# Kernel optimization log

Hardware: AMD Instinct MI355X
Metric: run time of the kernel (lower is better)

Reference implementation:

```python
import jax, jax.numpy as jnp
import numpy as np
from jax import lax

B, T, F, H, NC = 64, 256, 64, 128, 2


def setup_inputs() -> dict:
    key = jax.random.key(0)
    ks = jax.random.split(key, 10)
    # timestamps: sorted ints with duplicates -> exercises per-timestamp mean aggregation
    t = jnp.sort(jax.random.randint(ks[0], (B, T), 0, T // 2), axis=1).astype(jnp.float32)
    m = jax.random.randint(ks[1], (B, T), 0, F).astype(jnp.float32)
    x = jax.random.normal(ks[2], (B, T), dtype=jnp.float32)
    delt = jax.random.uniform(ks[3], (B, T), dtype=jnp.float32)
    X = jnp.stack([t, m, x, delt], axis=1)  # [B, 4, T]
    lengths = jax.random.randint(ks[4], (B,), T // 2, T + 1).astype(jnp.int32)
    s = 1.0 / np.sqrt(H + 1)
    W_lin = jax.random.uniform(ks[5], (F, H + 1, 4 * H), minval=-s, maxval=s, dtype=jnp.float32)
    b_lin = jax.random.uniform(ks[6], (F, 4 * H), minval=-s, maxval=s, dtype=jnp.float32)
    W_dec = jax.random.uniform(ks[7], (F,), minval=-1.0, maxval=1.0, dtype=jnp.float32)
    b_dec = jax.random.uniform(ks[8], (F,), minval=-1.0, maxval=1.0, dtype=jnp.float32)
    so = 1.0 / np.sqrt(F * H + H)
    k9, k10 = jax.random.split(ks[9])
    W_out = jax.random.uniform(k9, (F * H + H, NC), minval=-so, maxval=so, dtype=jnp.float32)
    b_out = jax.random.uniform(k10, (NC,), minval=-so, maxval=so, dtype=jnp.float32)
    return {"X": X, "lengths": lengths, "W_lin": W_lin, "b_lin": b_lin,
            "W_dec": W_dec, "b_dec": b_dec, "W_out": W_out, "b_out": b_out}


def _forward(X, lengths, W_lin, b_lin, W_dec, b_dec, W_out, b_out):
    nF, Hp1, H4 = W_lin.shape
    hs = Hp1 - 1
    t = X[:, 0]
    m = X[:, 1].astype(jnp.int32)
    x = X[:, 2]
    delt = X[:, 3]
    idx = jnp.arange(t.shape[1])
    valid = idx[None, :] < lengths[:, None]                       # event is real
    t_next = jnp.concatenate([t[:, 1:], t[:, -1:] + 1.0], axis=1)
    # last event of a consecutive-equal-timestamp group (within valid length)
    boundary = (idx[None, :] == (lengths[:, None] - 1)) | (t_next != t)

    def per_sample(m_s, x_s, d_s, v_s, b_s):
        def step(carry, inp):
            h_t, c_t, acc, cnt = carry
            mj, xj, dj, vj, bj = inp
            # feature-specific decay of that feature's hidden row
            dm = W_dec[mj] * dj + b_dec[mj]
            decay = jnp.exp(-jnp.maximum(0.0, dm))
            h_dec = decay * h_t[mj]
            inp_vec = jnp.concatenate([xj[None], h_dec])          # [H+1]
            gates = inp_vec @ W_lin[mj] + b_lin[mj]               # [4H]
            gi, gf, go, gc = jnp.split(gates, 4)
            c_cand = jax.nn.sigmoid(gf) * c_t + jax.nn.sigmoid(gi) * jnp.tanh(gc)
            h_row = jax.nn.sigmoid(go) * jnp.tanh(c_cand)
            h_t = jnp.where(vj, h_t.at[mj].set(h_row), h_t)
            acc = acc + jnp.where(vj, c_cand, 0.0)
            cnt = cnt + jnp.where(vj, 1.0, 0.0)
            close = vj & bj                                       # end of timestamp group
            c_t = jnp.where(close, acc / jnp.maximum(cnt, 1.0), c_t)
            acc = jnp.where(close, jnp.zeros_like(acc), acc)
            cnt = jnp.where(close, 0.0, cnt)
            return (h_t, c_t, acc, cnt), None

        init = (jnp.zeros((nF, hs), jnp.float32), jnp.zeros((hs,), jnp.float32),
                jnp.zeros((hs,), jnp.float32), jnp.float32(0.0))
        (h_t, c_t, _, _), _ = lax.scan(step, init, (m_s, x_s, d_s, v_s, b_s))
        feats = jnp.concatenate([c_t, h_t.reshape(-1)])           # [H + F*H]
        return jax.nn.softmax(feats @ W_out + b_out)

    return jax.vmap(per_sample)(m, x, delt, valid, boundary)      # [B, n_class]


def reference(X, lengths, W_lin, b_lin, W_dec, b_dec, W_out, b_out):
    return _forward(X, lengths, W_lin, b_lin, W_dec, b_dec, W_out, b_out)
```

## Files before the change

kernel.cpp:

```cpp
#include <hip/hip_runtime.h>
#include <math.h>
#include <stdint.h>

#define BATCH 64
#define T 256
#define NF 64
#define H 128
#define H4 512
#define HP1 129
#define WF_STRIDE (HP1 * H4)
#define FEATS (NF * H + H)
#define NTH3 1024

#define PACK2_U4 (64 * 8 * 2 * 4 * 64)
#define PACK2_BYTES ((size_t)PACK2_U4 * 16u)
#define HDR2_BYTES  (64u * 512u * 16u)
#define WS_NEED ((size_t)HDR2_BYTES + PACK2_BYTES)

typedef float vf2 __attribute__((ext_vector_type(2)));

__device__ __forceinline__ float sigmoidf_(float x) {
    return 1.0f / (1.0f + __expf(-x));
}

__device__ __forceinline__ float tanhf_(float x) {
    float ax = fabsf(x);
    float e = __expf(2.0f * ax);
    float r = 1.0f - 2.0f / (e + 1.0f);
    return copysignf(r, x);
}

template<bool HI>
__device__ __forceinline__ vf2 dec2f(unsigned u) {
    return __builtin_amdgcn_cvt_pk_f32_fp8(u, HI);
}

__global__ __launch_bounds__(256)
void repack2_kernel(const float* __restrict__ W_lin, uint4* __restrict__ pack2) {
    const int lin = blockIdx.x * 256 + threadIdx.x;
    const int l   = lin & 63;
    const int i   = (lin >> 6) & 3;
    const int Xv  = (lin >> 8) & 1;
    const int wv  = (lin >> 9) & 7;
    const int f   = lin >> 12;
    const int h   = wv * 16 + (l & 15);
    const int ks  = l >> 4;
    const int g   = Xv * 2 + (i >> 1);
    const int ksub = i & 1;
    const int col = g * 128 + h;
    const int k0  = ks * 32 + ksub * 16;
    const float* src = W_lin + (size_t)f * WF_STRIDE + (size_t)(1 + k0) * H4 + col;
    unsigned u[4];
    #pragma unroll
    for (int dw = 0; dw < 4; ++dw) {
        const float v0 = src[(4 * dw + 0) * H4] * 4096.0f;
        const float v1 = src[(4 * dw + 1) * H4] * 4096.0f;
        const float v2 = src[(4 * dw + 2) * H4] * 4096.0f;
        const float v3 = src[(4 * dw + 3) * H4] * 4096.0f;
        unsigned r = 0;
        r = __builtin_amdgcn_cvt_pk_fp8_f32(v0, v1, r, false);
        r = __builtin_amdgcn_cvt_pk_fp8_f32(v2, v3, r, true);
        u[dw] = r;
    }
    uint4 o; o.x = u[0]; o.y = u[1]; o.z = u[2]; o.w = u[3];
    pack2[lin] = o;
}

__global__ __launch_bounds__(256)
void hdr2_kernel(const float* __restrict__ W_lin, const float* __restrict__ b_lin,
                 uint4* __restrict__ hdr2) {
    const int lin = blockIdx.x * 256 + threadIdx.x;
    const int t2 = lin & 511, f = lin >> 9;
    const int wv = t2 >> 6, l = t2 & 63;
    const int h  = wv * 16 + (l & 15);
    union { uint4 u; _Float16 hf[8]; } o;
    #pragma unroll
    for (int g = 0; g < 4; ++g) {
        o.hf[g]     = (_Float16)W_lin[(size_t)f * WF_STRIDE + g * 128 + h];
        o.hf[4 + g] = (_Float16)b_lin[f * H4 + g * 128 + h];
    }
    hdr2[lin] = o.u;
}

__global__ __launch_bounds__(NTH3, 4)
void lstm_scan_fp8_pair(const float* __restrict__ X,
                        const int* __restrict__ lengths,
                        const float* __restrict__ W_dec,
                        const float* __restrict__ b_dec,
                        const float* __restrict__ W_out,
                        const float* __restrict__ b_out,
                        const uint4* __restrict__ pack2,
                        const uint4* __restrict__ hdr2,
                        float* __restrict__ out)
{
    __shared__ float s_ht[NF * H];
    __shared__ float s_inpA[H];
    __shared__ float s_inpB[H];
    __shared__ float s_gates[2][H][4];
    __shared__ float s_X[4 * T];
    __shared__ float s_wdec[NF];
    __shared__ float s_bdec[NF];
    __shared__ float s_cfin[H];
    __shared__ float s_red[32];

    const int tid = threadIdx.x;
    const int b   = blockIdx.x;
    const int grp = tid >> 9;
    const int w8  = (tid >> 6) & 7;
    const int l   = tid & 63;
    const int h   = w8 * 16 + (l & 15);
    const int ks  = l >> 4;

    const float* Xb = X + b * 4 * T;
    const int len = lengths[b];

    for (int i = tid; i < NF * H; i += NTH3) s_ht[i] = 0.0f;
    for (int i = tid; i < 4 * T; i += NTH3) s_X[i] = Xb[i];
    if (tid < NF) { s_wdec[tid] = W_dec[tid]; s_bdec[tid] = b_dec[tid]; }
    if (tid < H) { s_inpA[tid] = 0.0f; s_inpB[tid] = 0.0f; }
    __syncthreads();

    float c_t = 0.0f, accv = 0.0f, cntv = 0.0f;

    #define DOTQ(Wq, G, KS) do {                                                \
        const int pb = (KS) * 8;                                                \
        vf2 d;                                                                  \
        d = dec2f<false>((Wq).x); acc[G] += d * iv[pb + 0];                     \
        d = dec2f<true >((Wq).x); acc[G] += d * iv[pb + 1];                     \
        d = dec2f<false>((Wq).y); acc[G] += d * iv[pb + 2];                     \
        d = dec2f<true >((Wq).y); acc[G] += d * iv[pb + 3];                     \
        d = dec2f<false>((Wq).z); acc[G] += d * iv[pb + 4];                     \
        d = dec2f<true >((Wq).z); acc[G] += d * iv[pb + 5];                     \
        d = dec2f<false>((Wq).w); acc[G] += d * iv[pb + 6];                     \
        d = dec2f<true >((Wq).w); acc[G] += d * iv[pb + 7];                     \
    } while (0)

    #define MATVEC(MF, INP, XV, GATE) do {                                      \
        uint4 q[8];                                                             \
        const uint4* wp_ = pack2 + (((size_t)(MF) * 8 + w8) * 2 * 4) * 64 + l;  \
        _Pragma("unroll")                                                       \
        for (int ii = 0; ii < 8; ++ii) q[ii] = wp_[ii * 64];                    \
        union { uint4 u; _Float16 hf[8]; } hu_;                                 \
        hu_.u = hdr2[(size_t)(MF) * 512 + (w8 * 64 + l)];                       \
        vf2 iv[16];                                                             \
        {                                                                       \
            const float4* ip_ = (const float4*)((INP) + ks * 32);               \
            _Pragma("unroll")                                                   \
            for (int qd = 0; qd < 8; ++qd) {                                    \
                const float4 t_ = ip_[qd];                                      \
                iv[2 * qd][0] = t_.x;     iv[2 * qd][1] = t_.y;                 \
                iv[2 * qd + 1][0] = t_.z; iv[2 * qd + 1][1] = t_.w;             \
            }                                                                   \
        }                                                                       \
        vf2 acc[4];                                                             \
        _Pragma("unroll")                                                       \
        for (int g = 0; g < 4; ++g) { acc[g][0] = 0.0f; acc[g][1] = 0.0f; }     \
        _Pragma("unroll")                                                       \
        for (int Xi = 0; Xi < 2; ++Xi) {                                        \
            DOTQ(q[Xi * 4 + 0], Xi * 2 + 0, 0);                                 \
            DOTQ(q[Xi * 4 + 1], Xi * 2 + 0, 1);                                 \
            DOTQ(q[Xi * 4 + 2], Xi * 2 + 1, 0);                                 \
            DOTQ(q[Xi * 4 + 3], Xi * 2 + 1, 1);                                 \
        }                                                                       \
        _Pragma("unroll")                                                       \
        for (int g = 0; g < 4; ++g) {                                           \
            float s_ = acc[g][0] + acc[g][1];                                   \
            s_ += __shfl_xor(s_, 16, 64);                                       \
            s_ += __shfl_xor(s_, 32, 64);                                       \
            GATE[g] = fmaf(s_, 1.0f / 4096.0f,                                  \
                           fmaf((XV), (float)hu_.hf[g], (float)hu_.hf[4 + g])); \
        }                                                                       \
    } while (0)

    for (int j = 0; j < len; j += 2) {
        const int  vj1 = (j + 1 < len);
        const int  mj  = (int)s_X[T + j];
        const int  j1c = (j + 1 < T) ? (j + 1) : (T - 1);
        const int  mj1 = (int)s_X[T + j1c];
        const float xj  = s_X[2 * T + j];
        const float xj1 = s_X[2 * T + j1c];

        {
            const int   myM   = grp ? mj1 : mj;
            const float myx   = grp ? xj1 : xj;
            const float* myin = grp ? s_inpB : s_inpA;
            float gate[4];
            MATVEC(myM, myin, myx, gate);
            if (ks == 0) {
                float4 g4; g4.x = gate[0]; g4.y = gate[1]; g4.z = gate[2]; g4.w = gate[3];
                *(float4*)&s_gates[grp][h][0] = g4;
            }
        }
        __syncthreads();

        const float4 gA = *(const float4*)&s_gates[0][h][0];
        float4 gB = *(const float4*)&s_gates[1][h][0];

        const float c_candA = sigmoidf_(gA.y) * c_t + sigmoidf_(gA.x) * tanhf_(gA.w);
        const float h_rowA  = sigmoidf_(gA.z) * tanhf_(c_candA);
        accv += c_candA;
        cntv += 1.0f;
        {
            const float tj  = s_X[j];
            const float tn1 = (j < T - 1) ? s_X[j + 1] : (tj + 1.0f);
            const bool bdry = (j == len - 1) || (tn1 != tj);
            if (bdry) { c_t = accv / fmaxf(cntv, 1.0f); accv = 0.0f; cntv = 0.0f; }
        }

        const bool coll = vj1 && (mj1 == mj);
        if (coll) {
            const float d1  = s_X[3 * T + j1c];
            const float dm1 = fmaf(s_wdec[mj1], d1, s_bdec[mj1]);
            const float de1 = __expf(-fmaxf(0.0f, dm1));
            if (grp == 1 && ks == 0) s_inpB[h] = de1 * h_rowA;
            __syncthreads();
            if (grp == 1) {
                float gr[4];
                MATVEC(mj1, s_inpB, xj1, gr);
                if (ks == 0) {
                    float4 g4; g4.x = gr[0]; g4.y = gr[1]; g4.z = gr[2]; g4.w = gr[3];
                    *(float4*)&s_gates[1][h][0] = g4;
                }
            }
            __syncthreads();
            gB = *(const float4*)&s_gates[1][h][0];
        }

        float h_rowB = 0.0f;
        if (vj1) {
            const float c_candB = sigmoidf_(gB.y) * c_t + sigmoidf_(gB.x) * tanhf_(gB.w);
            h_rowB = sigmoidf_(gB.z) * tanhf_(c_candB);
            accv += c_candB;
            cntv += 1.0f;
            const float tj1 = s_X[j1c];
            const float tn2 = (j + 1 < T - 1) ? s_X[j + 2] : (tj1 + 1.0f);
            const bool bdry = (j + 1 == len - 1) || (tn2 != tj1);
            if (bdry) { c_t = accv / fmaxf(cntv, 1.0f); accv = 0.0f; cntv = 0.0f; }
        }

        if (ks == 0) {
            if (grp == 0 && !coll) s_ht[mj * H + h] = h_rowA;
            if (grp == 1 && vj1)   s_ht[mj1 * H + h] = h_rowB;
        }

        const int j2 = (j + 2 < T) ? (j + 2) : (T - 1);
        const int j3 = (j + 3 < T) ? (j + 3) : (T - 1);
        const int m2 = (int)s_X[T + j2];
        const int m3 = (int)s_X[T + j3];
        if (ks == 0 && grp == 0) {
            const float d2  = s_X[3 * T + j2];
            const float dm2 = fmaf(s_wdec[m2], d2, s_bdec[m2]);
            const float de2 = __expf(-fmaxf(0.0f, dm2));
            const float hv2 = (vj1 && m2 == mj1) ? h_rowB
                            : ((m2 == mj) ? h_rowA : s_ht[m2 * H + h]);
            s_inpA[h] = de2 * hv2;
        }
        if (ks == 0 && grp == 1) {
            const float d3  = s_X[3 * T + j3];
            const float dm3 = fmaf(s_wdec[m3], d3, s_bdec[m3]);
            const float de3 = __expf(-fmaxf(0.0f, dm3));
            const float hv3 = (vj1 && m3 == mj1) ? h_rowB
                            : ((m3 == mj) ? h_rowA : s_ht[m3 * H + h]);
            s_inpB[h] = de3 * hv3;
        }
        __syncthreads();
    }
    #undef MATVEC
    #undef DOTQ

    if (grp == 0 && ks == 0) s_cfin[h] = c_t;
    __syncthreads();

    float z0 = 0.0f, z1 = 0.0f;
    for (int i = tid; i < FEATS; i += NTH3) {
        const float f = (i < H) ? s_cfin[i] : s_ht[i - H];
        const float2 wo = *(const float2*)(W_out + 2 * i);
        z0 = fmaf(f, wo.x, z0);
        z1 = fmaf(f, wo.y, z1);
    }
    #pragma unroll
    for (int off = 32; off > 0; off >>= 1) {
        z0 += __shfl_down(z0, off, 64);
        z1 += __shfl_down(z1, off, 64);
    }
    const int wave = tid >> 6, lane2 = tid & 63;
    if (lane2 == 0) { s_red[2 * wave] = z0; s_red[2 * wave + 1] = z1; }
    __syncthreads();
    if (tid == 0) {
        float a0 = b_out[0], a1 = b_out[1];
        #pragma unroll
        for (int q = 0; q < 16; ++q) { a0 += s_red[2 * q]; a1 += s_red[2 * q + 1]; }
        const float mx = fmaxf(a0, a1);
        const float e0 = __expf(a0 - mx), e1 = __expf(a1 - mx);
        const float inv = 1.0f / (e0 + e1);
        out[2 * b]     = e0 * inv;
        out[2 * b + 1] = e1 * inv;
    }
}

#define NTHREADS 512
__global__ __launch_bounds__(NTHREADS)
void lstm_scan_kernel(const float* __restrict__ X,
                      const int* __restrict__ lengths,
                      const float* __restrict__ W_lin,
                      const float* __restrict__ b_lin,
                      const float* __restrict__ W_dec,
                      const float* __restrict__ b_dec,
                      const float* __restrict__ W_out,
                      const float* __restrict__ b_out,
                      float* __restrict__ out)
{
    __shared__ float s_feats[FEATS];
    __shared__ float s_inp[H];
    __shared__ float s_part[4][H4];
    __shared__ float s_X[4 * T];
    __shared__ float s_wdec[NF];
    __shared__ float s_bdec[NF];
    __shared__ float s_red[16];

    float* s_ct = s_feats;
    float* s_ht = s_feats + H;

    const int tid = threadIdx.x;
    const int b   = blockIdx.x;
    const int g4  = tid & 127;
    const int kq  = tid >> 7;

    const float* Xb = X + b * 4 * T;
    const int len = lengths[b];

    for (int i = tid; i < NF * H; i += NTHREADS) s_ht[i] = 0.0f;
    for (int i = tid; i < 4 * T; i += NTHREADS) s_X[i] = Xb[i];
    if (tid < NF) { s_wdec[tid] = W_dec[tid]; s_bdec[tid] = b_dec[tid]; }
    __syncthreads();

    float c_t = 0.0f, acc = 0.0f, cnt = 0.0f;

    for (int j = 0; j < len; ++j) {
        const int   mj = (int)s_X[T + j];
        const float xj = s_X[2 * T + j];
        const float* Wf = W_lin + mj * WF_STRIDE;

        float bl0, bl1, bl2, bl3;
        if (tid < H) {
            const float dj    = s_X[3 * T + j];
            const float dm    = fmaf(s_wdec[mj], dj, s_bdec[mj]);
            const float decay = __expf(-fmaxf(0.0f, dm));
            s_inp[tid] = decay * s_ht[mj * H + tid];
            const int m4 = mj * H4;
            bl0 = b_lin[m4 + tid];
            bl1 = b_lin[m4 + H + tid];
            bl2 = b_lin[m4 + 2 * H + tid];
            bl3 = b_lin[m4 + 3 * H + tid];
        }
        __syncthreads();

        float4 a4 = make_float4(0.0f, 0.0f, 0.0f, 0.0f);
        {
            const float*  wr  = Wf + (1 + kq * 32) * H4 + 4 * g4;
            const float4* ivp = (const float4*)(s_inp + kq * 32);
            #pragma unroll
            for (int cc = 0; cc < 8; ++cc) {
                const float4 v = ivp[cc];
                const float* wrc = wr + (4 * cc) * H4;
                const float4 w0 = *(const float4*)(wrc);
                const float4 w1 = *(const float4*)(wrc + H4);
                const float4 w2 = *(const float4*)(wrc + 2 * H4);
                const float4 w3 = *(const float4*)(wrc + 3 * H4);
                a4.x = fmaf(v.x, w0.x, a4.x); a4.y = fmaf(v.x, w0.y, a4.y);
                a4.z = fmaf(v.x, w0.z, a4.z); a4.w = fmaf(v.x, w0.w, a4.w);
                a4.x = fmaf(v.y, w1.x, a4.x); a4.y = fmaf(v.y, w1.y, a4.y);
                a4.z = fmaf(v.y, w1.z, a4.z); a4.w = fmaf(v.y, w1.w, a4.w);
                a4.x = fmaf(v.z, w2.x, a4.x); a4.y = fmaf(v.z, w2.y, a4.y);
                a4.z = fmaf(v.z, w2.z, a4.z); a4.w = fmaf(v.z, w2.w, a4.w);
                a4.x = fmaf(v.w, w3.x, a4.x); a4.y = fmaf(v.w, w3.y, a4.y);
                a4.z = fmaf(v.w, w3.z, a4.z); a4.w = fmaf(v.w, w3.w, a4.w);
            }
        }
        if (kq == 0) {
            const float4 wv = *(const float4*)(Wf + 4 * g4);
            a4.x = fmaf(xj, wv.x, a4.x); a4.y = fmaf(xj, wv.y, a4.y);
            a4.z = fmaf(xj, wv.z, a4.z); a4.w = fmaf(xj, wv.w, a4.w);
        }
        *(float4*)(&s_part[kq][4 * g4]) = a4;
        __syncthreads();

        if (tid < H) {
            const int h = tid;
            const float gi = s_part[0][h]         + s_part[1][h]         + s_part[2][h]         + s_part[3][h]         + bl0;
            const float gf = s_part[0][H + h]     + s_part[1][H + h]     + s_part[2][H + h]     + s_part[3][H + h]     + bl1;
            const float go = s_part[0][2*H + h]   + s_part[1][2*H + h]   + s_part[2][2*H + h]   + s_part[3][2*H + h]   + bl2;
            const float gc = s_part[0][3*H + h]   + s_part[1][3*H + h]   + s_part[2][3*H + h]   + s_part[3][3*H + h]   + bl3;

            const float c_cand = sigmoidf_(gf) * c_t + sigmoidf_(gi) * tanhf_(gc);
            const float h_row  = sigmoidf_(go) * tanhf_(c_cand);
            s_ht[mj * H + h] = h_row;
            acc += c_cand;
            cnt += 1.0f;

            const float tj = s_X[j];
            const float tn = (j < T - 1) ? s_X[j + 1] : (tj + 1.0f);
            const bool boundary = (j == len - 1) || (tn != tj);
            if (boundary) { c_t = acc / fmaxf(cnt, 1.0f); acc = 0.0f; cnt = 0.0f; }
        }
        __syncthreads();
    }

    if (tid < H) s_ct[tid] = c_t;
    __syncthreads();

    float z0 = 0.0f, z1 = 0.0f;
    for (int i = tid; i < FEATS; i += NTHREADS) {
        const float f = s_feats[i];
        const float2 wv = *(const float2*)(W_out + 2 * i);
        z0 = fmaf(f, wv.x, z0);
        z1 = fmaf(f, wv.y, z1);
    }
    #pragma unroll
    for (int off = 32; off > 0; off >>= 1) {
        z0 += __shfl_down(z0, off, 64);
        z1 += __shfl_down(z1, off, 64);
    }
    const int wave = tid >> 6, lane = tid & 63;
    if (lane == 0) { s_red[2 * wave] = z0; s_red[2 * wave + 1] = z1; }
    __syncthreads();
    if (tid == 0) {
        float a0 = b_out[0], a1 = b_out[1];
        #pragma unroll
        for (int q = 0; q < 8; ++q) { a0 += s_red[2 * q]; a1 += s_red[2 * q + 1]; }
        const float mx = fmaxf(a0, a1);
        const float e0 = __expf(a0 - mx), e1 = __expf(a1 - mx);
        const float inv = 1.0f / (e0 + e1);
        out[2 * b]     = e0 * inv;
        out[2 * b + 1] = e1 * inv;
    }
}

extern "C" void kernel_launch(void* const* d_in, const int* in_sizes, int n_in,
                              void* d_out, int out_size, void* d_ws, size_t ws_size,
                              hipStream_t stream) {
    const float* X      = (const float*)d_in[0];
    const int*   lens   = (const int*)d_in[1];
    const float* W_lin  = (const float*)d_in[2];
    const float* b_lin  = (const float*)d_in[3];
    const float* W_dec  = (const float*)d_in[4];
    const float* b_dec  = (const float*)d_in[5];
    const float* W_out  = (const float*)d_in[6];
    const float* b_out  = (const float*)d_in[7];
    float* out = (float*)d_out;

    if (ws_size >= WS_NEED) {
        uint4* hdr2 = (uint4*)d_ws;
        uint4* pack2 = (uint4*)((char*)d_ws + HDR2_BYTES);
        hipLaunchKernelGGL(hdr2_kernel, dim3(128), dim3(256), 0, stream,
                           W_lin, b_lin, hdr2);
        hipLaunchKernelGGL(repack2_kernel, dim3(PACK2_U4 / 256), dim3(256), 0, stream,
                           W_lin, pack2);
        hipLaunchKernelGGL(lstm_scan_fp8_pair, dim3(BATCH), dim3(NTH3), 0, stream,
                           X, lens, W_dec, b_dec, W_out, b_out, pack2, hdr2, out);
    } else {
        hipLaunchKernelGGL(lstm_scan_kernel, dim3(BATCH), dim3(NTHREADS), 0, stream,
                           X, lens, W_lin, b_lin, W_dec, b_dec, W_out, b_out, out);
    }
}
```

Baseline: 542.8 us.

## Prefetch next-step FP8 weights into LDS via async global_load_lds

The scan kernel now issues asynchronous global-to-LDS loads (global_load_lds) for the next step's feature weight slice while the current step computes, then reads weights from LDS with ds_read_b128 instead of loading them from global memory on the critical path. The hidden-state table moves to fp16 so the 128 KB weight staging buffer fits in shared memory, and __syncthreads is replaced by hand-written waitcnt/barrier macros. The aim is to hide global-memory latency in the serial per-timestep recurrence. In exchange it uses much more LDS, adds fp16 rounding to the stored hidden states, and depends on hand-placed waitcnt ordering being correct.

New measurement: 572.4 us. +5.5%, slower.

```diff
diff --git a/kernel.cpp b/kernel.cpp
--- a/kernel.cpp
+++ b/kernel.cpp
@@ -10,7 +10,7 @@
 #define HP1 129
 #define WF_STRIDE (HP1 * H4)
 #define FEATS (NF * H + H)
-#define NTH3 1024
+#define NTH4 1024
 
 #define PACK2_U4 (64 * 8 * 2 * 4 * 64)
 #define PACK2_BYTES ((size_t)PACK2_U4 * 16u)
@@ -34,6 +34,21 @@
 __device__ __forceinline__ vf2 dec2f(unsigned u) {
     return __builtin_amdgcn_cvt_pk_f32_fp8(u, HI);
 }
+
+__device__ __forceinline__ void dma16(const void* g, uint32_t lds_byte) {
+    __builtin_amdgcn_global_load_lds(
+        (const __attribute__((address_space(1))) void*)g,
+        (__attribute__((address_space(3))) void*)(uintptr_t)lds_byte,
+        16, 0, 0);
+}
+
+#define WAITV0() do { asm volatile("s_waitcnt vmcnt(0)" ::: "memory"); \
+                      __builtin_amdgcn_sched_barrier(0); } while (0)
+#define LGKM0()  do { asm volatile("s_waitcnt lgkmcnt(0)" ::: "memory"); \
+                      __builtin_amdgcn_sched_barrier(0); } while (0)
+#define BARRIER() do { asm volatile("s_waitcnt lgkmcnt(0)" ::: "memory"); \
+                       __builtin_amdgcn_s_barrier(); \
+                       asm volatile("" ::: "memory"); } while (0)
 
 __global__ __launch_bounds__(256)
 void repack2_kernel(const float* __restrict__ W_lin, uint4* __restrict__ pack2) {
@@ -82,22 +97,23 @@
     hdr2[lin] = o.u;
 }
 
-__global__ __launch_bounds__(NTH3, 4)
-void lstm_scan_fp8_pair(const float* __restrict__ X,
-                        const int* __restrict__ lengths,
-                        const float* __restrict__ W_dec,
-                        const float* __restrict__ b_dec,
-                        const float* __restrict__ W_out,
-                        const float* __restrict__ b_out,
-                        const uint4* __restrict__ pack2,
-                        const uint4* __restrict__ hdr2,
-                        float* __restrict__ out)
+__global__ __launch_bounds__(NTH4, 4)
+void lstm_scan_fp8_pair2(const float* __restrict__ X,
+                         const int* __restrict__ lengths,
+                         const float* __restrict__ W_dec,
+                         const float* __restrict__ b_dec,
+                         const float* __restrict__ W_out,
+                         const float* __restrict__ b_out,
+                         const uint4* __restrict__ pack2,
+                         const uint4* __restrict__ hdr2,
+                         float* __restrict__ out)
 {
-    __shared__ float s_ht[NF * H];
+    __shared__ __align__(16) char s_wb[131072];
+    __shared__ _Float16 s_ht[NF * H];
+    __shared__ __align__(16) float s_gates[2][H][4];
+    __shared__ float s_X[4 * T];
     __shared__ float s_inpA[H];
     __shared__ float s_inpB[H];
-    __shared__ float s_gates[2][H][4];
-    __shared__ float s_X[4 * T];
     __shared__ float s_wdec[NF];
     __shared__ float s_bdec[NF];
     __shared__ float s_cfin[H];
@@ -114,13 +130,24 @@
     const float* Xb = X + b * 4 * T;
     const int len = lengths[b];
 
-    for (int i = tid; i < NF * H; i += NTH3) s_ht[i] = 0.0f;
-    for (int i = tid; i < 4 * T; i += NTH3) s_X[i] = Xb[i];
+    for (int i = tid; i < NF * H; i += NTH4) s_ht[i] = (_Float16)0.0f;
+    for (int i = tid; i < 4 * T; i += NTH4) s_X[i] = Xb[i];
     if (tid < NF) { s_wdec[tid] = W_dec[tid]; s_bdec[tid] = b_dec[tid]; }
     if (tid < H) { s_inpA[tid] = 0.0f; s_inpB[tid] = 0.0f; }
     __syncthreads();
 
+    const uint32_t wb0 = (uint32_t)(uintptr_t)s_wb;
+    const uint32_t slice = __builtin_amdgcn_readfirstlane(
+        wb0 + (uint32_t)grp * 65536u + (uint32_t)w8 * 8192u);
+
     float c_t = 0.0f, accv = 0.0f, cntv = 0.0f;
+
+    #define ISSUE8(MF) do {                                                     \
+        const uint4* gp_ = pack2 + ((size_t)(MF) * 8 + w8) * 512 + l;           \
+        _Pragma("unroll")                                                       \
+        for (int ii = 0; ii < 8; ++ii)                                          \
+            dma16(gp_ + ii * 64, slice + (uint32_t)(ii * 1024));                \
+    } while (0)
 
     #define DOTQ(Wq, G, KS) do {                                                \
         const int pb = (KS) * 8;                                                \
@@ -135,13 +162,22 @@
         d = dec2f<true >((Wq).w); acc[G] += d * iv[pb + 7];                     \
     } while (0)
 
-    #define MATVEC(MF, INP, XV, GATE) do {                                      \
-        uint4 q[8];                                                             \
-        const uint4* wp_ = pack2 + (((size_t)(MF) * 8 + w8) * 2 * 4) * 64 + l;  \
-        _Pragma("unroll")                                                       \
-        for (int ii = 0; ii < 8; ++ii) q[ii] = wp_[ii * 64];                    \
-        union { uint4 u; _Float16 hf[8]; } hu_;                                 \
-        hu_.u = hdr2[(size_t)(MF) * 512 + (w8 * 64 + l)];                       \
+    #define MATVEC_LDS(INP, XV, HU, GATE) do {                                  \
+        uint4 q0, q1, q2, q3, q4, q5, q6, q7;                                   \
+        const uint32_t ra_ = wb0 + (uint32_t)grp * 65536u                       \
+                           + (uint32_t)w8 * 8192u + (uint32_t)l * 16u;          \
+        asm volatile("ds_read_b128 %0, %4 offset:0\n\t"                         \
+                     "ds_read_b128 %1, %4 offset:1024\n\t"                      \
+                     "ds_read_b128 %2, %4 offset:2048\n\t"                      \
+                     "ds_read_b128 %3, %4 offset:3072"                          \
+                     : "=&v"(q0), "=&v"(q1), "=&v"(q2), "=&v"(q3)               \
+                     : "v"(ra_) : "memory");                                    \
+        asm volatile("ds_read_b128 %0, %4 offset:4096\n\t"                      \
+                     "ds_read_b128 %1, %4 offset:5120\n\t"                      \
+                     "ds_read_b128 %2, %4 offset:6144\n\t"                      \
+                     "ds_read_b128 %3, %4 offset:7168"                          \
+                     : "=&v"(q4), "=&v"(q5), "=&v"(q6), "=&v"(q7)               \
+                     : "v"(ra_) : "memory");                                    \
         vf2 iv[16];                                                             \
         {                                                                       \
             const float4* ip_ = (const float4*)((INP) + ks * 32);               \
@@ -152,25 +188,27 @@
                 iv[2 * qd + 1][0] = t_.z; iv[2 * qd + 1][1] = t_.w;             \
             }                                                                   \
         }                                                                       \
+        LGKM0();          \
         vf2 acc[4];                                                             \
         _Pragma("unroll")                                                       \
         for (int g = 0; g < 4; ++g) { acc[g][0] = 0.0f; acc[g][1] = 0.0f; }     \
-        _Pragma("unroll")                                                       \
-        for (int Xi = 0; Xi < 2; ++Xi) {                                        \
-            DOTQ(q[Xi * 4 + 0], Xi * 2 + 0, 0);                                 \
-            DOTQ(q[Xi * 4 + 1], Xi * 2 + 0, 1);                                 \
-            DOTQ(q[Xi * 4 + 2], Xi * 2 + 1, 0);                                 \
-            DOTQ(q[Xi * 4 + 3], Xi * 2 + 1, 1);                                 \
-        }                                                                       \
+        DOTQ(q0, 0, 0); DOTQ(q1, 0, 1); DOTQ(q2, 1, 0); DOTQ(q3, 1, 1);         \
+        DOTQ(q4, 2, 0); DOTQ(q5, 2, 1); DOTQ(q6, 3, 0); DOTQ(q7, 3, 1);         \
         _Pragma("unroll")                                                       \
         for (int g = 0; g < 4; ++g) {                                           \
             float s_ = acc[g][0] + acc[g][1];                                   \
             s_ += __shfl_xor(s_, 16, 64);                                       \
             s_ += __shfl_xor(s_, 32, 64);                                       \
             GATE[g] = fmaf(s_, 1.0f / 4096.0f,                                  \
-                           fmaf((XV), (float)hu_.hf[g], (float)hu_.hf[4 + g])); \
+                           fmaf((XV), (float)(HU).hf[g], (float)(HU).hf[4 + g])); \
         }                                                                       \
     } while (0)
+
+    {
+        const int m0 = (int)s_X[T];
+        const int m1 = (int)s_X[T + ((1 < T) ? 1 : (T - 1))];
+        ISSUE8(grp ? m1 : m0);
+    }
 
     for (int j = 0; j < len; j += 2) {
         const int  vj1 = (j + 1 < len);
@@ -179,19 +217,32 @@
         const int  mj1 = (int)s_X[T + j1c];
         const float xj  = s_X[2 * T + j];
         const float xj1 = s_X[2 * T + j1c];
-
-        {
-            const int   myM   = grp ? mj1 : mj;
-            const float myx   = grp ? xj1 : xj;
-            const float* myin = grp ? s_inpB : s_inpA;
-            float gate[4];
-            MATVEC(myM, myin, myx, gate);
-            if (ks == 0) {
-                float4 g4; g4.x = gate[0]; g4.y = gate[1]; g4.z = gate[2]; g4.w = gate[3];
-                *(float4*)&s_gates[grp][h][0] = g4;
-            }
-        }
-        __syncthreads();
+        const bool coll = vj1 && (mj1 == mj);
+        const int  j2 = (j + 2 < T) ? (j + 2) : (T - 1);
+        const int  j3 = (j + 3 < T) ? (j + 3) : (T - 1);
+        const int  m2 = (int)s_X[T + j2];
+        const int  m3 = (int)s_X[T + j3];
+
+        const int   myM   = grp ? mj1 : mj;
+        const float myx   = grp ? xj1 : xj;
+        const float* myin = grp ? s_inpB : s_inpA;
+
+        union { uint4 u; _Float16 hf[8]; } hu;
+        hu.u = hdr2[(size_t)myM * 512 + (w8 * 64 + l)];
+
+        WAITV0();
+
+        float gate[4];
+        MATVEC_LDS(myin, myx, hu, gate);
+
+        if (grp == 0) ISSUE8(m2);
+        else if (!coll) ISSUE8(m3);
+
+        if (ks == 0) {
+            float4 g4; g4.x = gate[0]; g4.y = gate[1]; g4.z = gate[2]; g4.w = gate[3];
+            *(float4*)&s_gates[grp][h][0] = g4;
+        }
+        BARRIER();
 
         const float4 gA = *(const float4*)&s_gates[0][h][0];
         float4 gB = *(const float4*)&s_gates[1][h][0];
@@ -207,22 +258,22 @@
             if (bdry) { c_t = accv / fmaxf(cntv, 1.0f); accv = 0.0f; cntv = 0.0f; }
         }
 
-        const bool coll = vj1 && (mj1 == mj);
         if (coll) {
             const float d1  = s_X[3 * T + j1c];
             const float dm1 = fmaf(s_wdec[mj1], d1, s_bdec[mj1]);
             const float de1 = __expf(-fmaxf(0.0f, dm1));
             if (grp == 1 && ks == 0) s_inpB[h] = de1 * h_rowA;
-            __syncthreads();
+            BARRIER();
             if (grp == 1) {
                 float gr[4];
-                MATVEC(mj1, s_inpB, xj1, gr);
+                MATVEC_LDS(s_inpB, xj1, hu, gr);
+                ISSUE8(m3);
                 if (ks == 0) {
                     float4 g4; g4.x = gr[0]; g4.y = gr[1]; g4.z = gr[2]; g4.w = gr[3];
                     *(float4*)&s_gates[1][h][0] = g4;
                 }
             }
-            __syncthreads();
+            BARRIER();
             gB = *(const float4*)&s_gates[1][h][0];
         }
 
@@ -239,20 +290,16 @@
         }
 
         if (ks == 0) {
-            if (grp == 0 && !coll) s_ht[mj * H + h] = h_rowA;
-            if (grp == 1 && vj1)   s_ht[mj1 * H + h] = h_rowB;
-        }
-
-        const int j2 = (j + 2 < T) ? (j + 2) : (T - 1);
-        const int j3 = (j + 3 < T) ? (j + 3) : (T - 1);
-        const int m2 = (int)s_X[T + j2];
-        const int m3 = (int)s_X[T + j3];
+            if (grp == 0 && !coll) s_ht[mj * H + h] = (_Float16)h_rowA;
+            if (grp == 1 && vj1)   s_ht[mj1 * H + h] = (_Float16)h_rowB;
+        }
+
         if (ks == 0 && grp == 0) {
             const float d2  = s_X[3 * T + j2];
             const float dm2 = fmaf(s_wdec[m2], d2, s_bdec[m2]);
             const float de2 = __expf(-fmaxf(0.0f, dm2));
             const float hv2 = (vj1 && m2 == mj1) ? h_rowB
-                            : ((m2 == mj) ? h_rowA : s_ht[m2 * H + h]);
+                            : ((m2 == mj) ? h_rowA : (float)s_ht[m2 * H + h]);
             s_inpA[h] = de2 * hv2;
         }
         if (ks == 0 && grp == 1) {
@@ -260,20 +307,24 @@
             const float dm3 = fmaf(s_wdec[m3], d3, s_bdec[m3]);
             const float de3 = __expf(-fmaxf(0.0f, dm3));
             const float hv3 = (vj1 && m3 == mj1) ? h_rowB
-                            : ((m3 == mj) ? h_rowA : s_ht[m3 * H + h]);
+                            : ((m3 == mj) ? h_rowA : (float)s_ht[m3 * H + h]);
             s_inpB[h] = de3 * hv3;
         }
-        __syncthreads();
-    }
-    #undef MATVEC
+        BARRIER();
+    }
+    #undef MATVEC_LDS
     #undef DOTQ
+    #undef ISSUE8
+
+    asm volatile("s_waitcnt vmcnt(0) lgkmcnt(0)" ::: "memory");
+    __syncthreads();
 
     if (grp == 0 && ks == 0) s_cfin[h] = c_t;
     __syncthreads();
 
     float z0 = 0.0f, z1 = 0.0f;
-    for (int i = tid; i < FEATS; i += NTH3) {
-        const float f = (i < H) ? s_cfin[i] : s_ht[i - H];
+    for (int i = tid; i < FEATS; i += NTH4) {
+        const float f = (i < H) ? s_cfin[i] : (float)s_ht[i - H];
         const float2 wo = *(const float2*)(W_out + 2 * i);
         z0 = fmaf(f, wo.x, z0);
         z1 = fmaf(f, wo.y, z1);
@@ -456,7 +507,7 @@
                            W_lin, b_lin, hdr2);
         hipLaunchKernelGGL(repack2_kernel, dim3(PACK2_U4 / 256), dim3(256), 0, stream,
                            W_lin, pack2);
-        hipLaunchKernelGGL(lstm_scan_fp8_pair, dim3(BATCH), dim3(NTH3), 0, stream,
+        hipLaunchKernelGGL(lstm_scan_fp8_pair2, dim3(BATCH), dim3(NTH4), 0, stream,
                            X, lens, W_dec, b_dec, W_out, b_out, pack2, hdr2, out);
     } else {
         hipLaunchKernelGGL(lstm_scan_kernel, dim3(BATCH), dim3(NTHREADS), 0, stream,
```
